# Kernel tuning notes

Measured on AMD Instinct MI355X. Metric: run time of the kernel, lower is better.

## Reference

```python
import jax, jax.numpy as jnp
import numpy as np

IN_FEATURES = 4096
OUT_FEATURES = 11008
TOKENS = 8192


def setup_inputs() -> dict:
    key = jax.random.key(0)
    k_x, k_w, k_s, k_b = jax.random.split(key, 4)
    x = jax.random.normal(k_x, (TOKENS, IN_FEATURES), dtype=jnp.float32)
    # symmetric int8 weights in [-127, 127]
    qweight = jax.random.randint(k_w, (OUT_FEATURES, IN_FEATURES), -127, 128, dtype=jnp.int32).astype(jnp.int8)
    # per-output-channel positive scale (abs-max / 127 style)
    weight_scale = jax.random.uniform(k_s, (OUT_FEATURES, 1), dtype=jnp.float32, minval=1e-4, maxval=0.02)
    bias = jax.random.normal(k_b, (OUT_FEATURES,), dtype=jnp.float32)
    return {"x": x, "qweight": qweight, "weight_scale": weight_scale, "bias": bias}


def reference(x, qweight, weight_scale, bias):
    # dequantize: [out, in] fp weight = int8 * per-row scale, cast to x dtype
    weight = (qweight.astype(jnp.float32) * weight_scale).astype(x.dtype)
    # F.linear: x @ weight.T + bias
    out = jnp.einsum("ti,oi->to", x, weight) + bias.astype(x.dtype)
    return out
```

## Files before the change

### kernel.cpp

```cpp
#include <hip/hip_runtime.h>
#include <stdint.h>


#define TOKENS 8192
#define IN_F   4096
#define OUT_F  11008

#define BM 256
#define BN 256
#define BK 128
#define KT   (IN_F / BK)
#define MBLK (TOKENS / BM)
#define NBLK (OUT_F / BN)
#define NWG  (MBLK * NBLK)

static_assert(NWG % 8 == 0, "XCD swizzle requires nwg % 8 == 0");
static_assert(KT % 2 == 0, "double-buffer parity");

#define LDS_BUF   65536
#define LDS_TOTAL 131072

typedef __attribute__((ext_vector_type(4))) float f32x4;
typedef __attribute__((ext_vector_type(4))) int   i32x4;

__device__ __forceinline__ void gload_lds16(const void* g, void* l) {
  typedef const __attribute__((address_space(1))) unsigned int* gp_t;
  typedef __attribute__((address_space(3))) unsigned int* lp_t;
  __builtin_amdgcn_global_load_lds((gp_t)g, (lp_t)l, 16, 0, 0);
}

#define MFMA(d, a, b) \
  asm("v_mfma_i32_16x16x64_i8 %0, %1, %2, %0" : "+v"(d) : "v"(a), "v"(b))

#define BARRIER __builtin_amdgcn_s_barrier()
#define LGKM0                                                  \
  do {                                                         \
    asm volatile("s_waitcnt lgkmcnt(0)" ::: "memory");         \
    __builtin_amdgcn_sched_barrier(0);                         \
  } while (0)
#define VMW_(N) asm volatile("s_waitcnt vmcnt(" #N ")" ::: "memory")
#define VMW(N) VMW_(N)

__global__ __launch_bounds__(256) void quant_x_kernel(
    const float* __restrict__ x, signed char* __restrict__ xq,
    float* __restrict__ sx) {
  const int row = blockIdx.x;
  const int tid = threadIdx.x;
  const float* xr = x + (size_t)row * IN_F;
  f32x4 v[4];
#pragma unroll
  for (int p = 0; p < 4; ++p) v[p] = ((const f32x4*)xr)[tid + 256 * p];
  float am = 0.f;
#pragma unroll
  for (int p = 0; p < 4; ++p)
#pragma unroll
    for (int j = 0; j < 4; ++j) am = fmaxf(am, fabsf(v[p][j]));
#pragma unroll
  for (int off = 32; off; off >>= 1) am = fmaxf(am, __shfl_xor(am, off, 64));
  __shared__ float wmax[4];
  if ((tid & 63) == 0) wmax[tid >> 6] = am;
  __syncthreads();
  am = fmaxf(fmaxf(wmax[0], wmax[1]), fmaxf(wmax[2], wmax[3]));
  const float inv = (am > 0.f) ? 127.0f / am : 0.f;
  if (tid == 0) sx[row] = (am > 0.f) ? am / 127.0f : 1.0f;
  int* xqi = (int*)(xq + (size_t)row * IN_F);
#pragma unroll
  for (int p = 0; p < 4; ++p) {
    int pk = 0;
#pragma unroll
    for (int j = 0; j < 4; ++j) {
      int q = (int)rintf(v[p][j] * inv);
      pk |= (q & 0xff) << (8 * j);
    }
    xqi[tid + 256 * p] = pk;
  }
}

__global__ void cvt_w_kernel(const int* __restrict__ w,
                             signed char* __restrict__ wq, int n16) {
  int i = blockIdx.x * blockDim.x + threadIdx.x;
  int stride = gridDim.x * blockDim.x;
  for (int c = i; c < n16; c += stride) {
    const i32x4* src = (const i32x4*)w + (size_t)c * 4;
    i32x4 outv;
#pragma unroll
    for (int q = 0; q < 4; ++q) {
      i32x4 v = src[q];
      outv[q] = (v[0] & 0xff) | ((v[1] & 0xff) << 8) |
                ((v[2] & 0xff) << 16) | (v[3] << 24);
    }
    ((i32x4*)wq)[c] = outv;
  }
}

__global__ __launch_bounds__(512) void gemm_i8_kernel(
    const signed char* __restrict__ A,
    const signed char* __restrict__ Bm,
    const float* __restrict__ sx,
    const float* __restrict__ scale,
    const float* __restrict__ bias,
    float* __restrict__ C)
{
  extern __shared__ char lds[];

  const int tid  = threadIdx.x;
  const int lane = tid & 63;
  const int wave = tid >> 6;
  const int wm   = wave >> 2;
  const int wn   = wave & 3;
  const int grp  = lane >> 4;
  const int rsel = lane & 15;

  int bid = blockIdx.x;
  int wg  = (bid & 7) * (NWG / 8) + (bid >> 3);
  const int m_idx = wg % MBLK;
  const int n_idx = wg / MBLK;
  const int row0 = m_idx * BM;
  const int col0 = n_idx * BN;

  const int r0  = tid >> 3;
  const int jg  = (tid & 7) ^ (r0 & 7);
  const int gAL0 = r0;
  const int gAL1 = 128 + r0;
  const int gBL0 = r0 + (r0 & 32);
  const int gBL1 = 128 + r0 + (r0 & 32);
  const signed char* pAL0 = A  + (size_t)(row0 + gAL0) * IN_F + jg * 16;
  const signed char* pAL1 = A  + (size_t)(row0 + gAL1) * IN_F + jg * 16;
  const signed char* pAH0 = pAL0 + (size_t)64 * IN_F;
  const signed char* pAH1 = pAL1 + (size_t)64 * IN_F;
  const signed char* pBL0 = Bm + (size_t)(col0 + gBL0) * IN_F + jg * 16;
  const signed char* pBL1 = Bm + (size_t)(col0 + gBL1) * IN_F + jg * 16;
  const signed char* pBH0 = pBL0 + (size_t)32 * IN_F;
  const signed char* pBH1 = pBL1 + (size_t)32 * IN_F;
  const int stBase = wave * 1024;

  auto stALBL = [&](int bo, int t2) {
    const int ko = t2 * BK;
    gload_lds16(pAL0 + ko, lds + bo + 0     + stBase);
    gload_lds16(pAL1 + ko, lds + bo + 8192  + stBase);
    gload_lds16(pBL0 + ko, lds + bo + 32768 + stBase);
    gload_lds16(pBL1 + ko, lds + bo + 40960 + stBase);
  };
  auto stBH = [&](int bo, int t2) {
    const int ko = t2 * BK;
    gload_lds16(pBH0 + ko, lds + bo + 49152 + stBase);
    gload_lds16(pBH1 + ko, lds + bo + 57344 + stBase);
  };
  auto stAH = [&](int bo, int t2) {
    const int ko = t2 * BK;
    gload_lds16(pAH0 + ko, lds + bo + 16384 + stBase);
    gload_lds16(pAH1 + ko, lds + bo + 24576 + stBase);
  };

  const int swz0  = (grp ^ (rsel & 7)) << 4;
  const int swz1  = swz0 ^ 64;
  const int aBase = wm * 8192 + rsel * 128;
  const int bBase = wn * 4096 + rsel * 128;

  i32x4 zero = {0, 0, 0, 0};
  i32x4 acc[8][4];
#pragma unroll
  for (int m = 0; m < 8; ++m)
#pragma unroll
    for (int n = 0; n < 4; ++n) acc[m][n] = zero;

#define DS_AL(BO, MI, SW) (*(const i32x4*)(lds + (BO) + 0     + aBase + (MI)*2048 + (SW)))
#define DS_AH(BO, MI, SW) (*(const i32x4*)(lds + (BO) + 16384 + aBase + (MI)*2048 + (SW)))
#define DS_BL(BO, NI, SW) (*(const i32x4*)(lds + (BO) + 32768 + bBase + (NI)*2048 + (SW)))
#define DS_BH(BO, NI, SW) (*(const i32x4*)(lds + (BO) + 49152 + bBase + (NI)*2048 + (SW)))

#define TILE(BO, T, DO_STAGE, W0, W1, W3)                                      \
  {                                                                            \
    i32x4 arLo[8], arHi[8], brLo[4], brHi[4];                                  \
                                          \
    _Pragma("unroll") for (int m = 0; m < 4; ++m) {                            \
      arLo[m * 2]     = DS_AL(BO, m, swz0);                                    \
      arLo[m * 2 + 1] = DS_AL(BO, m, swz1);                                    \
    }                                                                          \
    _Pragma("unroll") for (int n = 0; n < 2; ++n) {                            \
      brLo[n * 2]     = DS_BL(BO, n, swz0);                                    \
      brLo[n * 2 + 1] = DS_BL(BO, n, swz1);                                    \
    }                                                                          \
    BARRIER;                                                                   \
    LGKM0;                                                                     \
    __builtin_amdgcn_s_setprio(1);                                             \
    _Pragma("unroll") for (int m = 0; m < 4; ++m)                              \
      _Pragma("unroll") for (int n = 0; n < 2; ++n)                            \
        _Pragma("unroll") for (int kk = 0; kk < 2; ++kk)                       \
          MFMA(acc[m][n], arLo[m * 2 + kk], brLo[n * 2 + kk]);                 \
    __builtin_amdgcn_s_setprio(0);                                             \
    VMW(W0);                                                                   \
    BARRIER;                                                                   \
                               \
    _Pragma("unroll") for (int n = 0; n < 2; ++n) {                            \
      brHi[n * 2]     = DS_BH(BO, n, swz0);                                    \
      brHi[n * 2 + 1] = DS_BH(BO, n, swz1);                                    \
    }                                                                          \
    if (DO_STAGE) stALBL((BO), (T) + 2);                                       \
    BARRIER;                                                                   \
    LGKM0;                                                                     \
    __builtin_amdgcn_s_setprio(1);                                             \
    _Pragma("unroll") for (int m = 0; m < 4; ++m)                              \
      _Pragma("unroll") for (int n = 0; n < 2; ++n)                            \
        _Pragma("unroll") for (int kk = 0; kk < 2; ++kk)                       \
          MFMA(acc[m][n + 2], arLo[m * 2 + kk], brHi[n * 2 + kk]);             \
    __builtin_amdgcn_s_setprio(0);                                             \
    VMW(W1);                                                                   \
    BARRIER;                                                                   \
                                  \
    _Pragma("unroll") for (int m = 0; m < 4; ++m) {                            \
      arHi[m * 2]     = DS_AH(BO, m, swz0);                                    \
      arHi[m * 2 + 1] = DS_AH(BO, m, swz1);                                    \
    }                                                                          \
    if (DO_STAGE) stBH((BO), (T) + 2);                                         \
    BARRIER;                                                                   \
    LGKM0;                                                                     \
    __builtin_amdgcn_s_setprio(1);                                             \
    _Pragma("unroll") for (int m = 0; m < 4; ++m)                              \
      _Pragma("unroll") for (int n = 0; n < 2; ++n)                            \
        _Pragma("unroll") for (int kk = 0; kk < 2; ++kk)                       \
          MFMA(acc[m + 4][n + 2], arHi[m * 2 + kk], brHi[n * 2 + kk]);         \
    __builtin_amdgcn_s_setprio(0);                                             \
    BARRIER;                                                                   \
                        \
    if (DO_STAGE) stAH((BO), (T) + 2);                                         \
    __builtin_amdgcn_s_setprio(1);                                             \
    _Pragma("unroll") for (int m = 0; m < 4; ++m)                              \
      _Pragma("unroll") for (int n = 0; n < 2; ++n)                            \
        _Pragma("unroll") for (int kk = 0; kk < 2; ++kk)                       \
          MFMA(acc[m + 4][n], arHi[m * 2 + kk], brLo[n * 2 + kk]);             \
    __builtin_amdgcn_s_setprio(0);                                             \
    VMW(W3);                                                                   \
    BARRIER;                                                                   \
  }

  stALBL(0, 0);        stBH(0, 0);        stAH(0, 0);
  stALBL(LDS_BUF, 1);  stBH(LDS_BUF, 1);  stAH(LDS_BUF, 1);
  VMW(12);
  BARRIER;

  for (int t2 = 0; t2 < KT - 2; t2 += 2) {
    TILE(0,       t2,     true, 10, 12, 12);
    TILE(LDS_BUF, t2 + 1, true, 10, 12, 12);
  }
  TILE(0,       KT - 2, false, 10, 8, 4);
  TILE(LDS_BUF, KT - 1, false, 2, 0, 0);

#undef TILE
#undef DS_AL
#undef DS_AH
#undef DS_BL
#undef DS_BH

  asm volatile("s_nop 7\n\ts_nop 7" :::);

#pragma unroll
  for (int n = 0; n < 4; ++n) {
    int o = col0 + wn * 64 + n * 16 + rsel;
    float s  = scale[o];
    float bz = bias[o];
#pragma unroll
    for (int m = 0; m < 8; ++m) {
      int tr = row0 + wm * 128 + m * 16 + grp * 4;
      const f32x4 sxv = *(const f32x4*)(sx + tr);
      float* cp = C + (size_t)tr * OUT_F + o;
      i32x4 v = acc[m][n];
      cp[0 * (size_t)OUT_F] = (float)v[0] * (sxv[0] * s) + bz;
      cp[1 * (size_t)OUT_F] = (float)v[1] * (sxv[1] * s) + bz;
      cp[2 * (size_t)OUT_F] = (float)v[2] * (sxv[2] * s) + bz;
      cp[3 * (size_t)OUT_F] = (float)v[3] * (sxv[3] * s) + bz;
    }
  }
}

__global__ void gemm_naive_kernel(const float* __restrict__ x,
                                  const int* __restrict__ w,
                                  const float* __restrict__ sc,
                                  const float* __restrict__ bs,
                                  float* __restrict__ out) {
  long long idx = (long long)blockIdx.x * blockDim.x + threadIdx.x;
  long long total = (long long)TOKENS * OUT_F;
  if (idx >= total) return;
  int t = (int)(idx / OUT_F);
  int o = (int)(idx % OUT_F);
  const float* xp = x + (size_t)t * IN_F;
  const int* wp = w + (size_t)o * IN_F;
  float acc = 0.f;
  for (int k = 0; k < IN_F; k += 4) {
    i32x4 wv = *(const i32x4*)(wp + k);
    f32x4 xv = *(const f32x4*)(xp + k);
    acc += xv[0] * (float)wv[0] + xv[1] * (float)wv[1]
         + xv[2] * (float)wv[2] + xv[3] * (float)wv[3];
  }
  out[idx] = acc * sc[o] + bs[o];
}

extern "C" void kernel_launch(void* const* d_in, const int* in_sizes, int n_in,
                              void* d_out, int out_size, void* d_ws, size_t ws_size,
                              hipStream_t stream) {
  const float* x  = (const float*)d_in[0];
  const int*   qw = (const int*)d_in[1];
  const float* sc = (const float*)d_in[2];
  const float* bs = (const float*)d_in[3];
  float* out = (float*)d_out;

  const size_t xqBytes = (size_t)TOKENS * IN_F;
  const size_t wqBytes = (size_t)OUT_F * IN_F;
  const size_t sxBytes = (size_t)TOKENS * sizeof(float);

  if (ws_size >= xqBytes + wqBytes + sxBytes) {
    signed char* xq = (signed char*)d_ws;
    signed char* wq = (signed char*)((char*)d_ws + xqBytes);
    float*       sx = (float*)((char*)d_ws + xqBytes + wqBytes);
    quant_x_kernel<<<TOKENS, 256, 0, stream>>>(x, xq, sx);
    cvt_w_kernel<<<2048, 256, 0, stream>>>(qw, wq, OUT_F * IN_F / 16);
    (void)hipFuncSetAttribute((const void*)gemm_i8_kernel,
                              hipFuncAttributeMaxDynamicSharedMemorySize,
                              LDS_TOTAL);
    gemm_i8_kernel<<<NWG, 512, LDS_TOTAL, stream>>>(xq, wq, sx, sc, bs, out);
  } else {
    long long total = (long long)TOKENS * OUT_F;
    int blocks = (int)((total + 255) / 256);
    gemm_naive_kernel<<<blocks, 256, 0, stream>>>(x, qw, sc, bs, out);
  }
}
```

Before: 520.0 us.

## Software-pipeline LDS fragment reads across tiles with partial lgkmcnt waits

Restructures the int8 GEMM main loop so that LDS fragment reads for the next quadrant, and the next tile's A-lo/B fragments, are issued before the current MFMA block. The full lgkmcnt(0) waits become partial ones, letting ds_reads overlap MFMA work. Even and odd tiles use a serpentine quadrant order so fragments already in registers are reused, and staging of the global-to-LDS loads is split into finer pieces with retuned vmcnt thresholds. Launch bounds now request 2 blocks per CU. This may raise register pressure or cause spills, and the hand-tuned wait counts are fragile.

```diff
diff --git a/kernel.cpp b/kernel.cpp
--- a/kernel.cpp
+++ b/kernel.cpp
@@ -33,11 +33,12 @@
   asm("v_mfma_i32_16x16x64_i8 %0, %1, %2, %0" : "+v"(d) : "v"(a), "v"(b))
 
 #define BARRIER __builtin_amdgcn_s_barrier()
-#define LGKM0                                                  \
+#define LGKMC_(N)                                              \
   do {                                                         \
-    asm volatile("s_waitcnt lgkmcnt(0)" ::: "memory");         \
+    asm volatile("s_waitcnt lgkmcnt(" #N ")" ::: "memory");    \
     __builtin_amdgcn_sched_barrier(0);                         \
   } while (0)
+#define LGKMC(N) LGKMC_(N)
 #define VMW_(N) asm volatile("s_waitcnt vmcnt(" #N ")" ::: "memory")
 #define VMW(N) VMW_(N)
 
@@ -93,7 +94,7 @@
   }
 }
 
-__global__ __launch_bounds__(512) void gemm_i8_kernel(
+__global__ __launch_bounds__(512, 2) void gemm_i8_kernel(
     const signed char* __restrict__ A,
     const signed char* __restrict__ Bm,
     const float* __restrict__ sx,
@@ -134,10 +135,18 @@
   const signed char* pBH1 = pBL1 + (size_t)32 * IN_F;
   const int stBase = wave * 1024;
 
-  auto stALBL = [&](int bo, int t2) {
+  auto stAL = [&](int bo, int t2) {
     const int ko = t2 * BK;
     gload_lds16(pAL0 + ko, lds + bo + 0     + stBase);
     gload_lds16(pAL1 + ko, lds + bo + 8192  + stBase);
+  };
+  auto stAH = [&](int bo, int t2) {
+    const int ko = t2 * BK;
+    gload_lds16(pAH0 + ko, lds + bo + 16384 + stBase);
+    gload_lds16(pAH1 + ko, lds + bo + 24576 + stBase);
+  };
+  auto stBL = [&](int bo, int t2) {
+    const int ko = t2 * BK;
     gload_lds16(pBL0 + ko, lds + bo + 32768 + stBase);
     gload_lds16(pBL1 + ko, lds + bo + 40960 + stBase);
   };
@@ -146,11 +155,6 @@
     gload_lds16(pBH0 + ko, lds + bo + 49152 + stBase);
     gload_lds16(pBH1 + ko, lds + bo + 57344 + stBase);
   };
-  auto stAH = [&](int bo, int t2) {
-    const int ko = t2 * BK;
-    gload_lds16(pAH0 + ko, lds + bo + 16384 + stBase);
-    gload_lds16(pAH1 + ko, lds + bo + 24576 + stBase);
-  };
 
   const int swz0  = (grp ^ (rsel & 7)) << 4;
   const int swz1  = swz0 ^ 64;
@@ -164,93 +168,125 @@
 #pragma unroll
     for (int n = 0; n < 4; ++n) acc[m][n] = zero;
 
+  i32x4 arLo[8], arHi[8], brLo[4], brHi[4];
+
 #define DS_AL(BO, MI, SW) (*(const i32x4*)(lds + (BO) + 0     + aBase + (MI)*2048 + (SW)))
 #define DS_AH(BO, MI, SW) (*(const i32x4*)(lds + (BO) + 16384 + aBase + (MI)*2048 + (SW)))
 #define DS_BL(BO, NI, SW) (*(const i32x4*)(lds + (BO) + 32768 + bBase + (NI)*2048 + (SW)))
 #define DS_BH(BO, NI, SW) (*(const i32x4*)(lds + (BO) + 49152 + bBase + (NI)*2048 + (SW)))
 
-#define TILE(BO, T, DO_STAGE, W0, W1, W3)                                      \
+#define RD_ARLO(BO)                                                            \
+  _Pragma("unroll") for (int m = 0; m < 4; ++m) {                              \
+    arLo[m * 2]     = DS_AL(BO, m, swz0);                                      \
+    arLo[m * 2 + 1] = DS_AL(BO, m, swz1);                                      \
+  }
+#define RD_ARHI(BO)                                                            \
+  _Pragma("unroll") for (int m = 0; m < 4; ++m) {                              \
+    arHi[m * 2]     = DS_AH(BO, m, swz0);                                      \
+    arHi[m * 2 + 1] = DS_AH(BO, m, swz1);                                      \
+  }
+#define RD_BRLO(BO)                                                            \
+  _Pragma("unroll") for (int n = 0; n < 2; ++n) {                              \
+    brLo[n * 2]     = DS_BL(BO, n, swz0);                                      \
+    brLo[n * 2 + 1] = DS_BL(BO, n, swz1);                                      \
+  }
+#define RD_BRHI(BO)                                                            \
+  _Pragma("unroll") for (int n = 0; n < 2; ++n) {                              \
+    brHi[n * 2]     = DS_BH(BO, n, swz0);                                      \
+    brHi[n * 2 + 1] = DS_BH(BO, n, swz1);                                      \
+  }
+
+#define MM_Q00                                                                 \
+  _Pragma("unroll") for (int m = 0; m < 4; ++m)                                \
+    _Pragma("unroll") for (int n = 0; n < 2; ++n)                              \
+      _Pragma("unroll") for (int kk = 0; kk < 2; ++kk)                         \
+        MFMA(acc[m][n], arLo[m * 2 + kk], brLo[n * 2 + kk]);
+#define MM_Q01                                                                 \
+  _Pragma("unroll") for (int m = 0; m < 4; ++m)                                \
+    _Pragma("unroll") for (int n = 0; n < 2; ++n)                              \
+      _Pragma("unroll") for (int kk = 0; kk < 2; ++kk)                         \
+        MFMA(acc[m][n + 2], arLo[m * 2 + kk], brHi[n * 2 + kk]);
+#define MM_Q11                                                                 \
+  _Pragma("unroll") for (int m = 0; m < 4; ++m)                                \
+    _Pragma("unroll") for (int n = 0; n < 2; ++n)                              \
+      _Pragma("unroll") for (int kk = 0; kk < 2; ++kk)                         \
+        MFMA(acc[m + 4][n + 2], arHi[m * 2 + kk], brHi[n * 2 + kk]);
+#define MM_Q10                                                                 \
+  _Pragma("unroll") for (int m = 0; m < 4; ++m)                                \
+    _Pragma("unroll") for (int n = 0; n < 2; ++n)                              \
+      _Pragma("unroll") for (int kk = 0; kk < 2; ++kk)                         \
+        MFMA(acc[m + 4][n], arHi[m * 2 + kk], brLo[n * 2 + kk]);
+
+#define PRIO1 __builtin_amdgcn_s_setprio(1)
+#define PRIO0 __builtin_amdgcn_s_setprio(0)
+
+#define TILE_EVEN(BO, T, STG, W0, W2, W3)                                      \
   {                                                                            \
-    i32x4 arLo[8], arHi[8], brLo[4], brHi[4];                                  \
-                                          \
-    _Pragma("unroll") for (int m = 0; m < 4; ++m) {                            \
-      arLo[m * 2]     = DS_AL(BO, m, swz0);                                    \
-      arLo[m * 2 + 1] = DS_AL(BO, m, swz1);                                    \
-    }                                                                          \
-    _Pragma("unroll") for (int n = 0; n < 2; ++n) {                            \
-      brLo[n * 2]     = DS_BL(BO, n, swz0);                                    \
-      brLo[n * 2 + 1] = DS_BL(BO, n, swz1);                                    \
-    }                                                                          \
+    RD_BRHI(BO);                                                               \
+    LGKMC(4);                                                                  \
+    PRIO1; MM_Q00; PRIO0;                                                      \
+    VMW(W0); BARRIER;                                                          \
+    RD_ARHI(BO);                                                               \
+    if (STG) { stAL((BO), (T) + 2); stBL((BO), (T) + 2); }                     \
+    LGKMC(8);                                                                  \
+    PRIO1; MM_Q01; PRIO0;                                                      \
     BARRIER;                                                                   \
-    LGKM0;                                                                     \
-    __builtin_amdgcn_s_setprio(1);                                             \
-    _Pragma("unroll") for (int m = 0; m < 4; ++m)                              \
-      _Pragma("unroll") for (int n = 0; n < 2; ++n)                            \
-        _Pragma("unroll") for (int kk = 0; kk < 2; ++kk)                       \
-          MFMA(acc[m][n], arLo[m * 2 + kk], brLo[n * 2 + kk]);                 \
-    __builtin_amdgcn_s_setprio(0);                                             \
-    VMW(W0);                                                                   \
+    if (STG) stBH((BO), (T) + 2);                                              \
+    LGKMC(0);                                                                  \
+    PRIO1; MM_Q11; PRIO0;                                                      \
+    VMW(W2); BARRIER;                                                          \
+    RD_ARLO((BO) ^ LDS_BUF);                                                   \
+    RD_BRHI((BO) ^ LDS_BUF);                                                   \
+    if (STG) stAH((BO), (T) + 2);                                              \
+    LGKMC(12);                                                                 \
+    PRIO1; MM_Q10; PRIO0;                                                      \
+    VMW(W3); BARRIER;                                                          \
+  }
+
+#define TILE_ODD(BO, T, STG, RDN, W0, W2, W3, LG3)                             \
+  {                                                                            \
+    RD_BRLO(BO);                                                               \
+    LGKMC(4);                                                                  \
+    PRIO1; MM_Q01; PRIO0;                                                      \
+    VMW(W0); BARRIER;                                                          \
+    RD_ARHI(BO);                                                               \
+    if (STG) { stAL((BO), (T) + 2); stBH((BO), (T) + 2); }                     \
+    LGKMC(8);                                                                  \
+    PRIO1; MM_Q00; PRIO0;                                                      \
     BARRIER;                                                                   \
-                               \
-    _Pragma("unroll") for (int n = 0; n < 2; ++n) {                            \
-      brHi[n * 2]     = DS_BH(BO, n, swz0);                                    \
-      brHi[n * 2 + 1] = DS_BH(BO, n, swz1);                                    \
-    }                                                                          \
-    if (DO_STAGE) stALBL((BO), (T) + 2);                                       \
-    BARRIER;                                                                   \
-    LGKM0;                                                                     \
-    __builtin_amdgcn_s_setprio(1);                                             \
-    _Pragma("unroll") for (int m = 0; m < 4; ++m)                              \
-      _Pragma("unroll") for (int n = 0; n < 2; ++n)                            \
-        _Pragma("unroll") for (int kk = 0; kk < 2; ++kk)                       \
-          MFMA(acc[m][n + 2], arLo[m * 2 + kk], brHi[n * 2 + kk]);             \
-    __builtin_amdgcn_s_setprio(0);                                             \
-    VMW(W1);                                                                   \
-    BARRIER;                                                                   \
-                                  \
-    _Pragma("unroll") for (int m = 0; m < 4; ++m) {                            \
-      arHi[m * 2]     = DS_AH(BO, m, swz0);                                    \
-      arHi[m * 2 + 1] = DS_AH(BO, m, swz1);                                    \
-    }                                                                          \
-    if (DO_STAGE) stBH((BO), (T) + 2);                                         \
-    BARRIER;                                                                   \
-    LGKM0;                                                                     \
-    __builtin_amdgcn_s_setprio(1);                                             \
-    _Pragma("unroll") for (int m = 0; m < 4; ++m)                              \
-      _Pragma("unroll") for (int n = 0; n < 2; ++n)                            \
-        _Pragma("unroll") for (int kk = 0; kk < 2; ++kk)                       \
-          MFMA(acc[m + 4][n + 2], arHi[m * 2 + kk], brHi[n * 2 + kk]);         \
-    __builtin_amdgcn_s_setprio(0);                                             \
-    BARRIER;                                                                   \
-                        \
-    if (DO_STAGE) stAH((BO), (T) + 2);                                         \
-    __builtin_amdgcn_s_setprio(1);                                             \
-    _Pragma("unroll") for (int m = 0; m < 4; ++m)                              \
-      _Pragma("unroll") for (int n = 0; n < 2; ++n)                            \
-        _Pragma("unroll") for (int kk = 0; kk < 2; ++kk)                       \
-          MFMA(acc[m + 4][n], arHi[m * 2 + kk], brLo[n * 2 + kk]);             \
-    __builtin_amdgcn_s_setprio(0);                                             \
-    VMW(W3);                                                                   \
-    BARRIER;                                                                   \
-  }
-
-  stALBL(0, 0);        stBH(0, 0);        stAH(0, 0);
-  stALBL(LDS_BUF, 1);  stBH(LDS_BUF, 1);  stAH(LDS_BUF, 1);
+    if (STG) stBL((BO), (T) + 2);                                              \
+    LGKMC(0);                                                                  \
+    PRIO1; MM_Q10; PRIO0;                                                      \
+    VMW(W2); BARRIER;                                                          \
+    if (RDN) { RD_ARLO((BO) ^ LDS_BUF); RD_BRLO((BO) ^ LDS_BUF); }             \
+    if (STG) stAH((BO), (T) + 2);                                              \
+    LGKMC(LG3);                                                                \
+    PRIO1; MM_Q11; PRIO0;                                                      \
+    VMW(W3); BARRIER;                                                          \
+  }
+
+  stAL(0, 0); stBL(0, 0);
+  stBH(0, 0);
+  stAH(0, 0);
+  stAL(LDS_BUF, 1); stBH(LDS_BUF, 1);
+  stBL(LDS_BUF, 1);
+  stAH(LDS_BUF, 1);
   VMW(12);
   BARRIER;
+  RD_ARLO(0);
+  RD_BRLO(0);
+  VMW(10);
+  BARRIER;
 
   for (int t2 = 0; t2 < KT - 2; t2 += 2) {
-    TILE(0,       t2,     true, 10, 12, 12);
-    TILE(LDS_BUF, t2 + 1, true, 10, 12, 12);
-  }
-  TILE(0,       KT - 2, false, 10, 8, 4);
-  TILE(LDS_BUF, KT - 1, false, 2, 0, 0);
-
-#undef TILE
-#undef DS_AL
-#undef DS_AH
-#undef DS_BL
-#undef DS_BH
+    TILE_EVEN(0, t2, 1, 8, 10, 10);
+    TILE_ODD(LDS_BUF, t2 + 1, 1, 1, 8, 10, 10, 12);
+  }
+  TILE_EVEN(0, KT - 2, 0, 8, 4, 2);
+  TILE_ODD(LDS_BUF, KT - 1, 0, 0, 0, 0, 0, 0);
+
+#undef TILE_EVEN
+#undef TILE_ODD
 
   asm volatile("s_nop 7\n\ts_nop 7" :::);
 
```

After: 936.0 us. 1.8x slower.
